# Performance work log

Hardware: AMD Instinct MI355X
Metric: run time of the kernel (lower is better)

Reference implementation:

```python
import jax, jax.numpy as jnp
import numpy as np

B, S, D = 64, 196, 768   # batch, patch-seq, emb_dim
H = 12                   # attention heads
DH = D // H              # 64 per-head dim
HID = 3072               # MLP hidden
NUM_CLASSES = 1000
NUM_ENC = 4              # encoder applied NUM_ENC times with SHARED weights
POS_VOCAB = 201          # nn.Embedding(200+1, D)
EPS = 1e-5


def setup_inputs() -> dict:
    key = jax.random.key(0)
    ks = jax.random.split(key, 16)
    std = 0.02
    return {
        "image": jax.random.normal(ks[0], (B, S, D), jnp.float32),
        "clstoken": jax.random.normal(ks[1], (1, 1, D), jnp.float32),
        "pos_emb": jax.random.normal(ks[2], (POS_VOCAB, D), jnp.float32) * std,
        "ln1_g": jnp.ones((D,), jnp.float32),
        "ln1_b": jnp.zeros((D,), jnp.float32),
        # weights stored [in, out] so y = x @ W (equivalent to torch Linear)
        "wq": jax.random.normal(ks[3], (D, D), jnp.float32) * std,
        "wk": jax.random.normal(ks[4], (D, D), jnp.float32) * std,
        "wv": jax.random.normal(ks[5], (D, D), jnp.float32) * std,
        "ln2_g": jnp.ones((D,), jnp.float32),
        "ln2_b": jnp.zeros((D,), jnp.float32),
        "w1": jax.random.normal(ks[6], (D, HID), jnp.float32) * std,
        "b1": jnp.zeros((HID,), jnp.float32),
        "w2": jax.random.normal(ks[7], (HID, D), jnp.float32) * std,
        "b2": jnp.zeros((D,), jnp.float32),
        "head_w": jax.random.normal(ks[8], (D, NUM_CLASSES), jnp.float32) * std,
        "head_b": jnp.zeros((NUM_CLASSES,), jnp.float32),
    }


def _layernorm(x, g, b):
    mu = jnp.mean(x, axis=-1, keepdims=True)
    var = jnp.mean(jnp.square(x - mu), axis=-1, keepdims=True)
    return (x - mu) * jax.lax.rsqrt(var + EPS) * g + b


def _attention(x, wq, wk, wv):
    b, s, _ = x.shape
    def split_heads(t):  # (b, s, D) -> (b, H, s, DH)
        return t.reshape(b, s, H, DH).transpose(0, 2, 1, 3)
    q = split_heads(x @ wq)
    k = split_heads(x @ wk)
    v = split_heads(x @ wv)
    scores = jnp.einsum("bhqd,bhkd->bhqk", q, k) / np.sqrt(DH).astype(np.float32)
    probs = jax.nn.softmax(scores, axis=-1)
    out = jnp.einsum("bhqk,bhkd->bhqd", probs, v)
    return out.transpose(0, 2, 1, 3).reshape(b, s, D)  # no output projection (as in source)


def _encoder(x, ln1_g, ln1_b, wq, wk, wv, ln2_g, ln2_b, w1, b1, w2, b2):
    a = x + _attention(_layernorm(x, ln1_g, ln1_b), wq, wk, wv)
    h = _layernorm(a, ln2_g, ln2_b)
    mlp = jax.nn.relu(h @ w1 + b1) @ w2 + b2
    return a + mlp


def reference(image, clstoken, pos_emb, ln1_g, ln1_b, wq, wk, wv,
              ln2_g, ln2_b, w1, b1, w2, b2, head_w, head_b):
    b = image.shape[0]
    cls = jnp.broadcast_to(clstoken, (b, 1, D))
    x = jnp.concatenate([cls, image], axis=1)          # (b, S+1, D)
    x = x + pos_emb[: x.shape[1]][None, :, :]           # positional embeddings
    for _ in range(NUM_ENC):                            # shared weights across layers
        x = _encoder(x, ln1_g, ln1_b, wq, wk, wv, ln2_g, ln2_b, w1, b1, w2, b2)
    return x[:, 0, :] @ head_w + head_b                 # (b, num_classes)
```

## Files before the change

### kernel.cpp

```cpp
#include <hip/hip_runtime.h>
#include <hip/hip_bf16.h>
#include <stdint.h>


typedef __attribute__((ext_vector_type(8))) short bf16x8;
typedef __attribute__((ext_vector_type(4))) short bf16x4;
typedef __attribute__((ext_vector_type(4))) float f32x4;

#define LOG2E 1.44269504088896340736f

typedef const __attribute__((address_space(1))) uint32_t gas_u32;
typedef __attribute__((address_space(3))) uint32_t las_u32;

__device__ __forceinline__ void gld_lds16(const void* g, void* l) {
  __builtin_amdgcn_global_load_lds((gas_u32*)g, (las_u32*)l, 16, 0, 0);
}

__device__ __forceinline__ bf16x8 lds_read8u(const __hip_bfloat16* p) {
  union { bf16x4 h[2]; bf16x8 v; } u;
  u.h[0] = *(const bf16x4*)p;
  u.h[1] = *(const bf16x4*)(p + 4);
  return u.v;
}

__device__ __forceinline__ float ldin(const void* p, size_t i, int bf) {
  return bf ? __bfloat162float(((const __hip_bfloat16*)p)[i])
            : ((const float*)p)[i];
}

__device__ __forceinline__ float4 ldin4(const void* p, size_t i4, int bf) {
  if (bf) {
    union { uint2 u; __hip_bfloat16 e[4]; } v;
    v.u = *(const uint2*)((const __hip_bfloat16*)p + i4 * 4);
    return make_float4(__bfloat162float(v.e[0]), __bfloat162float(v.e[1]),
                       __bfloat162float(v.e[2]), __bfloat162float(v.e[3]));
  }
  return ((const float4*)p)[i4];
}

__global__ void k_flag(const void* __restrict__ g, int* __restrict__ flag) {
  if (threadIdx.x == 0 && blockIdx.x == 0) {
    uint32_t w = *(const uint32_t*)g;
    *flag = ((w & 0xFFFFu) == 0x3F80u) ? 1 : 0;
  }
}

__global__ __launch_bounds__(256) void k_embed(
    const void* __restrict__ img, const void* __restrict__ cls,
    const void* __restrict__ pos, float* __restrict__ X,
    const int* __restrict__ dflag)
{
  const int bf = *dflag;
  size_t idx4 = (size_t)blockIdx.x * 256 + threadIdx.x;
  if (idx4 >= (size_t)12608 * 192) return;
  int d4 = (int)(idx4 % 192);
  int row = (int)(idx4 / 192);
  int b = row / 197, s = row % 197;
  float4 base = (s == 0) ? ldin4(cls, d4, bf)
                         : ldin4(img, (size_t)(b * 196 + s - 1) * 192 + d4, bf);
  float4 p = ldin4(pos, (size_t)s * 192 + d4, bf);
  ((float4*)X)[idx4] = make_float4(base.x + p.x, base.y + p.y, base.z + p.z, base.w + p.w);
}

__global__ __launch_bounds__(256) void k_packT(
    const void* __restrict__ in, __hip_bfloat16* __restrict__ out,
    int K, int N, int NR, const int* __restrict__ dflag)
{
  __shared__ float t[32][33];
  const int bf = *dflag;
  int ktiles = (K + 31) >> 5;
  int k0 = (blockIdx.x % ktiles) << 5;
  int n0 = (blockIdx.x / ktiles) << 5;
  int tx = threadIdx.x & 31, ty = threadIdx.x >> 5;
#pragma unroll
  for (int i = 0; i < 32; i += 8) {
    int k = k0 + ty + i, n = n0 + tx;
    t[ty + i][tx] = (k < K && n < N) ? ldin(in, (size_t)k * N + n, bf) : 0.f;
  }
  __syncthreads();
#pragma unroll
  for (int i = 0; i < 32; i += 8) {
    int n = n0 + ty + i, k = k0 + tx;
    if (n < NR && k < K)
      out[(size_t)n * K + k] = __float2bfloat16(t[tx][ty + i]);
  }
}

__global__ __launch_bounds__(256) void k_packcls(
    const float* __restrict__ X, __hip_bfloat16* __restrict__ xcls)
{
  int idx = blockIdx.x * 256 + threadIdx.x;
  if (idx >= 128 * 768) return;
  int r = idx / 768, d = idx % 768;
  float v = (r < 64) ? X[(size_t)r * 197 * 768 + d] : 0.f;
  xcls[idx] = __float2bfloat16(v);
}

__global__ __launch_bounds__(256) void k_ln(
    const float* __restrict__ X, const void* __restrict__ g,
    const void* __restrict__ b, __hip_bfloat16* __restrict__ Y, int rows,
    const int* __restrict__ dflag)
{
  const int bf = *dflag;
  int wave = threadIdx.x >> 6, lane = threadIdx.x & 63;
  int row = blockIdx.x * 4 + wave;
  if (row >= rows) return;
  const float4* xr = (const float4*)(X + (size_t)row * 768);
  float4 v[3];
  float s = 0.f;
#pragma unroll
  for (int i = 0; i < 3; i++) {
    v[i] = xr[lane + i * 64];
    s += v[i].x + v[i].y + v[i].z + v[i].w;
  }
#pragma unroll
  for (int m = 1; m < 64; m <<= 1) s += __shfl_xor(s, m, 64);
  float mu = s * (1.f / 768.f);
  float q = 0.f;
#pragma unroll
  for (int i = 0; i < 3; i++) {
    float dx = v[i].x - mu, dy = v[i].y - mu, dz = v[i].z - mu, dw = v[i].w - mu;
    q += dx * dx + dy * dy + dz * dz + dw * dw;
  }
#pragma unroll
  for (int m = 1; m < 64; m <<= 1) q += __shfl_xor(q, m, 64);
  float rs = rsqrtf(q * (1.f / 768.f) + 1e-5f);
  uint2* yr = (uint2*)(Y + (size_t)row * 768);
#pragma unroll
  for (int i = 0; i < 3; i++) {
    int i4 = lane + i * 64;
    float4 gv = ldin4(g, i4, bf);
    float4 bv = ldin4(b, i4, bf);
    union { uint2 u; __hip_bfloat16 e[4]; } o;
    o.e[0] = __float2bfloat16((v[i].x - mu) * rs * gv.x + bv.x);
    o.e[1] = __float2bfloat16((v[i].y - mu) * rs * gv.y + bv.y);
    o.e[2] = __float2bfloat16((v[i].z - mu) * rs * gv.z + bv.z);
    o.e[3] = __float2bfloat16((v[i].w - mu) * rs * gv.w + bv.w);
    yr[i4] = o.u;
  }
}

template <int EPI>
__global__ __launch_bounds__(256, 2) void k_gemm(
    const __hip_bfloat16* __restrict__ A, const __hip_bfloat16* __restrict__ Bt,
    const void* __restrict__ bias, const float* __restrict__ Res,
    void* __restrict__ Cout, int K, int N, int Mstore, int ntiles,
    const int* __restrict__ dflag)
{
  __shared__ __align__(16) __hip_bfloat16 As[128 * 32];
  __shared__ __align__(16) __hip_bfloat16 Bs[128 * 32];

  const int bf = (EPI == 0) ? 0 : *dflag;
  const int tid = threadIdx.x;
  const int bm = blockIdx.x / ntiles;
  const int bn = blockIdx.x % ntiles;
  const int m0 = bm * 128, n0 = bn * 128;
  const int wave = tid >> 6, lane = tid & 63;
  const int wm = (wave >> 1) * 64, wn = (wave & 1) * 64;
  const int qd = lane >> 4, l16 = lane & 15;

  const int r0 = tid >> 2, kk0 = (tid & 3) * 8;
  const __hip_bfloat16* Ag0 = A + (size_t)(m0 + r0) * K + kk0;
  const __hip_bfloat16* Ag1 = A + (size_t)(m0 + r0 + 64) * K + kk0;
  const __hip_bfloat16* Bg0 = Bt + (size_t)(n0 + r0) * K + kk0;
  const __hip_bfloat16* Bg1 = Bt + (size_t)(n0 + r0 + 64) * K + kk0;
  __hip_bfloat16* As0 = &As[tid * 8];
  __hip_bfloat16* As1 = &As[(tid + 256) * 8];
  __hip_bfloat16* Bs0 = &Bs[tid * 8];
  __hip_bfloat16* Bs1 = &Bs[(tid + 256) * 8];

  f32x4 acc[4][4] = {};

  for (int k0 = 0; k0 < K; k0 += 32) {
    gld_lds16(Ag0, As0); gld_lds16(Ag1, As1);
    gld_lds16(Bg0, Bs0); gld_lds16(Bg1, Bs1);
    Ag0 += 32; Ag1 += 32; Bg0 += 32; Bg1 += 32;
    __syncthreads();
    bf16x8 af[4], bfr[4];
#pragma unroll
    for (int i = 0; i < 4; i++)
      af[i] = *(const bf16x8*)&As[(wm + i * 16 + l16) * 32 + qd * 8];
#pragma unroll
    for (int j = 0; j < 4; j++)
      bfr[j] = *(const bf16x8*)&Bs[(wn + j * 16 + l16) * 32 + qd * 8];
#pragma unroll
    for (int i = 0; i < 4; i++)
#pragma unroll
      for (int j = 0; j < 4; j++)
        acc[i][j] = __builtin_amdgcn_mfma_f32_16x16x32_bf16(af[i], bfr[j], acc[i][j], 0, 0, 0);
    __syncthreads();
  }

#pragma unroll
  for (int i = 0; i < 4; i++) {
#pragma unroll
    for (int r = 0; r < 4; r++) {
      int gr = m0 + wm + i * 16 + qd * 4 + r;
      if (gr < Mstore) {
#pragma unroll
        for (int j = 0; j < 4; j++) {
          int gc = n0 + wn + j * 16 + l16;
          float v = acc[i][j][r];
          if (EPI == 0) {
            ((__hip_bfloat16*)Cout)[(size_t)gr * N + gc] = __float2bfloat16(v);
          } else if (EPI == 1) {
            v += ldin(bias, gc, bf);
            v = v > 0.f ? v : 0.f;
            ((__hip_bfloat16*)Cout)[(size_t)gr * N + gc] = __float2bfloat16(v);
          } else if (EPI == 2) {
            v += ldin(bias, gc, bf) + Res[(size_t)gr * N + gc];
            ((float*)Cout)[(size_t)gr * N + gc] = v;
          } else {
            if (gc < N) {
              v += ldin(bias, gc, bf);
              if (bf) ((__hip_bfloat16*)Cout)[(size_t)gr * N + gc] = __float2bfloat16(v);
              else    ((float*)Cout)[(size_t)gr * N + gc] = v;
            }
          }
        }
      }
    }
  }
}

__global__ __launch_bounds__(256, 2) void k_attn(
    const __hip_bfloat16* __restrict__ qkv,
    const float* __restrict__ X, float* __restrict__ Aout)
{
  const int half = blockIdx.x & 1;
  const int bh = blockIdx.x >> 1;
  const int b = bh / 12, h = bh % 12;
  const size_t tokbase = (size_t)b * 197;

  __shared__ __align__(16) __hip_bfloat16 Ks[128 * 68];
  __shared__ __align__(16) __hip_bfloat16 Vt[64 * 132];
  __shared__ __align__(16) __hip_bfloat16 Ps[4][16 * 132];

  const int tid = threadIdx.x;
  const int wave = tid >> 6, lane = tid & 63;
  const int qd = lane >> 4, l16 = lane & 15;

  const int tbase = half * 7;
  const int tcnt = half ? 6 : 7;
  const int mt[2] = { tbase + wave, tbase + wave + 4 };
  const int nmt = (wave + 4 < tcnt) ? 2 : 1;

  f32x4 Ofr[2][4] = {};
  float mrun[2][4], lrun[2][4];
#pragma unroll
  for (int i = 0; i < 2; i++)
#pragma unroll
    for (int r = 0; r < 4; r++) { mrun[i][r] = -1e30f; lrun[i][r] = 0.f; }

  for (int jt = 0; jt < 2; jt++) {
    const int j0 = jt * 128;
    for (int c = tid; c < 128 * 16; c += 256) {
      int j = c >> 4, ch = (c & 15) * 4;
      const __hip_bfloat16* ksrc = qkv + (tokbase + j0 + j) * 2304 + 768 + h * 64 + ch;
      *(uint2*)&Ks[j * 68 + ch] = *(const uint2*)ksrc;
      const __hip_bfloat16* vsrc = qkv + (tokbase + j0 + j) * 2304 + 1536 + h * 64 + ch;
      union { uint2 u; __hip_bfloat16 e[4]; } vv;
      vv.u = *(const uint2*)vsrc;
      bool jvalid = (j0 + j) < 197;
      __hip_bfloat16 zero = __float2bfloat16(0.f);
#pragma unroll
      for (int i = 0; i < 4; i++)
        Vt[(ch + i) * 132 + j] = jvalid ? vv.e[i] : zero;
    }
    __syncthreads();

#pragma unroll
    for (int im = 0; im < 2; im++) {
      if (im < nmt) {
        const int m0 = mt[im] * 16;
        const __hip_bfloat16* qsrc = qkv + (tokbase + m0 + l16) * 2304 + h * 64 + qd * 8;
        bf16x8 qa0 = *(const bf16x8*)qsrc;
        bf16x8 qa1 = *(const bf16x8*)(qsrc + 32);

        f32x4 sc[8];
#pragma unroll
        for (int nt = 0; nt < 8; nt++) {
          bf16x8 kb0 = lds_read8u(&Ks[(nt * 16 + l16) * 68 + qd * 8]);
          bf16x8 kb1 = lds_read8u(&Ks[(nt * 16 + l16) * 68 + 32 + qd * 8]);
          f32x4 t = {0.f, 0.f, 0.f, 0.f};
          t = __builtin_amdgcn_mfma_f32_16x16x32_bf16(qa0, kb0, t, 0, 0, 0);
          sc[nt] = __builtin_amdgcn_mfma_f32_16x16x32_bf16(qa1, kb1, t, 0, 0, 0);
        }

        float rmax[4];
#pragma unroll
        for (int r = 0; r < 4; r++) rmax[r] = mrun[im][r];
#pragma unroll
        for (int nt = 0; nt < 8; nt++) {
          int col = j0 + nt * 16 + l16;
          bool valid = col < 197;
#pragma unroll
          for (int r = 0; r < 4; r++) {
            float sv = valid ? fminf(fmaxf(sc[nt][r] * 0.125f, -1e30f), 1e30f) : -1e30f;
            sc[nt][r] = sv;
            rmax[r] = fmaxf(rmax[r], sv);
          }
        }
#pragma unroll
        for (int r = 0; r < 4; r++) {
          float v = rmax[r];
          v = fmaxf(v, __shfl_xor(v, 1, 64));
          v = fmaxf(v, __shfl_xor(v, 2, 64));
          v = fmaxf(v, __shfl_xor(v, 4, 64));
          v = fmaxf(v, __shfl_xor(v, 8, 64));
          rmax[r] = v;
        }
        float alpha[4], rsum[4];
#pragma unroll
        for (int r = 0; r < 4; r++) {
          alpha[r] = exp2f((mrun[im][r] - rmax[r]) * LOG2E);
          rsum[r] = 0.f;
        }
#pragma unroll
        for (int nt = 0; nt < 8; nt++) {
#pragma unroll
          for (int r = 0; r < 4; r++) {
            float p = exp2f((sc[nt][r] - rmax[r]) * LOG2E);
            rsum[r] += p;
            Ps[wave][(qd * 4 + r) * 132 + nt * 16 + l16] = __float2bfloat16(p);
          }
        }
#pragma unroll
        for (int r = 0; r < 4; r++) {
          float v = rsum[r];
          v += __shfl_xor(v, 1, 64);
          v += __shfl_xor(v, 2, 64);
          v += __shfl_xor(v, 4, 64);
          v += __shfl_xor(v, 8, 64);
          lrun[im][r] = lrun[im][r] * alpha[r] + v;
          mrun[im][r] = rmax[r];
#pragma unroll
          for (int dt = 0; dt < 4; dt++) Ofr[im][dt][r] *= alpha[r];
        }

#pragma unroll
        for (int kf = 0; kf < 4; kf++) {
          bf16x8 pa = lds_read8u(&Ps[wave][l16 * 132 + kf * 32 + qd * 8]);
#pragma unroll
          for (int dt = 0; dt < 4; dt++) {
            bf16x8 vb = lds_read8u(&Vt[(dt * 16 + l16) * 132 + kf * 32 + qd * 8]);
            Ofr[im][dt] = __builtin_amdgcn_mfma_f32_16x16x32_bf16(pa, vb, Ofr[im][dt], 0, 0, 0);
          }
        }
      }
    }
    __syncthreads();
  }

#pragma unroll
  for (int im = 0; im < 2; im++) {
    if (im < nmt) {
      const int m0 = mt[im] * 16;
#pragma unroll
      for (int r = 0; r < 4; r++) {
        int row = m0 + qd * 4 + r;
        if (row < 197) {
          float inv = 1.f / lrun[im][r];
          size_t gbase = (tokbase + row) * 768 + h * 64;
#pragma unroll
          for (int dt = 0; dt < 4; dt++) {
            int col = dt * 16 + l16;
            Aout[gbase + col] = X[gbase + col] + Ofr[im][dt][r] * inv;
          }
        }
      }
    }
  }
}

extern "C" void kernel_launch(void* const* d_in, const int* in_sizes, int n_in,
                              void* d_out, int out_size, void* d_ws, size_t ws_size,
                              hipStream_t stream)
{
  const void* image = d_in[0];
  const void* cls   = d_in[1];
  const void* pos   = d_in[2];
  const void* ln1g  = d_in[3];
  const void* ln1b  = d_in[4];
  const void* wq    = d_in[5];
  const void* wk    = d_in[6];
  const void* wv    = d_in[7];
  const void* ln2g  = d_in[8];
  const void* ln2b  = d_in[9];
  const void* w1    = d_in[10];
  const void* b1    = d_in[11];
  const void* w2    = d_in[12];
  const void* b2    = d_in[13];
  const void* hw    = d_in[14];
  const void* hb    = d_in[15];

  if (ws_size < 188157952ull) return;

  char* w = (char*)d_ws;
  __hip_bfloat16* xn    = (__hip_bfloat16*)(w);
  __hip_bfloat16* qkv   = (__hip_bfloat16*)(w + 19464192);
  __hip_bfloat16* hid   = qkv;
  __hip_bfloat16* hwT   = qkv;
  __hip_bfloat16* xcls  = (__hip_bfloat16*)(w + 19464192 + 1572864);
  __hip_bfloat16* wqkvT = (__hip_bfloat16*)(w + 97320960);
  __hip_bfloat16* w1T   = (__hip_bfloat16*)(w + 100859904);
  __hip_bfloat16* w2T   = (__hip_bfloat16*)(w + 105578496);
  float* X              = (float*)(w + 110297088);
  float* A              = (float*)(w + 149225472);
  int* dflag            = (int*)(w + 188153856);

  k_flag<<<1, 64, 0, stream>>>(ln1g, dflag);
  k_packT<<<24 * 24, 256, 0, stream>>>(wq, wqkvT,             768,  768,  768, dflag);
  k_packT<<<24 * 24, 256, 0, stream>>>(wk, wqkvT +  768 * 768, 768,  768,  768, dflag);
  k_packT<<<24 * 24, 256, 0, stream>>>(wv, wqkvT + 1536 * 768, 768,  768,  768, dflag);
  k_packT<<<24 * 96, 256, 0, stream>>>(w1, w1T,                768, 3072, 3072, dflag);
  k_packT<<<96 * 24, 256, 0, stream>>>(w2, w2T,               3072,  768,  768, dflag);
  k_embed<<<9456, 256, 0, stream>>>(image, cls, pos, X, dflag);

  for (int l = 0; l < 4; l++) {
    k_ln<<<3152, 256, 0, stream>>>(X, ln1g, ln1b, xn, 12608, dflag);
    k_gemm<0><<<99 * 18, 256, 0, stream>>>(xn, wqkvT, (const void*)nullptr,
                                           (const float*)nullptr, qkv, 768, 2304, 12608, 18, dflag);
    k_attn<<<1536, 256, 0, stream>>>(qkv, X, A);
    k_ln<<<3152, 256, 0, stream>>>(A, ln2g, ln2b, xn, 12608, dflag);
    k_gemm<1><<<99 * 24, 256, 0, stream>>>(xn, w1T, b1, (const float*)nullptr,
                                           hid, 768, 3072, 12608, 24, dflag);
    k_gemm<2><<<99 * 6, 256, 0, stream>>>(hid, w2T, b2, A, X, 3072, 768, 12608, 6, dflag);
  }

  k_packT<<<24 * 32, 256, 0, stream>>>(hw, hwT, 768, 1000, 1024, dflag);
  k_packcls<<<384, 256, 0, stream>>>(X, xcls);
  k_gemm<3><<<8, 256, 0, stream>>>(xcls, hwT, hb, (const float*)nullptr,
                                   d_out, 768, 1000, 64, 8, dflag);
}
```

Measured before the change: 1.601 ms.

## Swizzle GEMM LDS layout and remap blocks to XCDs for L2 reuse

Applies an XOR swizzle to the k-chunk position within each LDS row of the A and B tiles, so the 16-byte fragment reads for MFMA spread across banks instead of conflicting. Remaps block IDs so that consecutive blocks scheduled round-robin across the 8 XCDs share M-tiles within an XCD, which is meant to improve L2 reuse of A rows and weight tiles. The grid is padded to 8*13 M-tiles, and the extra blocks exit early.

```diff
diff --git a/kernel.cpp b/kernel.cpp
--- a/kernel.cpp
+++ b/kernel.cpp
@@ -140,26 +140,37 @@
   }
 }
 
-template <int EPI>
+template <int EPI, int ORDER>
 __global__ __launch_bounds__(256, 2) void k_gemm(
     const __hip_bfloat16* __restrict__ A, const __hip_bfloat16* __restrict__ Bt,
     const void* __restrict__ bias, const float* __restrict__ Res,
-    void* __restrict__ Cout, int K, int N, int Mstore, int ntiles,
+    void* __restrict__ Cout, int K, int N, int Mstore, int ntiles, int mtiles,
     const int* __restrict__ dflag)
 {
   __shared__ __align__(16) __hip_bfloat16 As[128 * 32];
   __shared__ __align__(16) __hip_bfloat16 Bs[128 * 32];
 
+  int bm, bn;
+  if (ORDER == 2) {
+    bm = blockIdx.x / ntiles; bn = blockIdx.x % ntiles;
+  } else {
+    const int xcd = blockIdx.x & 7;
+    const int i = blockIdx.x >> 3;
+    if (ORDER == 0) { bn = i / 13; bm = xcd * 13 + (i % 13); }
+    else            { bm = xcd * 13 + i / ntiles; bn = i % ntiles; }
+    if (bm >= mtiles) return;
+  }
+
   const int bf = (EPI == 0) ? 0 : *dflag;
   const int tid = threadIdx.x;
-  const int bm = blockIdx.x / ntiles;
-  const int bn = blockIdx.x % ntiles;
   const int m0 = bm * 128, n0 = bn * 128;
   const int wave = tid >> 6, lane = tid & 63;
   const int wm = (wave >> 1) * 64, wn = (wave & 1) * 64;
   const int qd = lane >> 4, l16 = lane & 15;
 
-  const int r0 = tid >> 2, kk0 = (tid & 3) * 8;
+  const int r0 = tid >> 2;
+  const int sw0 = (r0 >> 1) & 3;
+  const int kk0 = ((tid & 3) ^ sw0) * 8;
   const __hip_bfloat16* Ag0 = A + (size_t)(m0 + r0) * K + kk0;
   const __hip_bfloat16* Ag1 = A + (size_t)(m0 + r0 + 64) * K + kk0;
   const __hip_bfloat16* Bg0 = Bt + (size_t)(n0 + r0) * K + kk0;
@@ -178,11 +189,15 @@
     __syncthreads();
     bf16x8 af[4], bfr[4];
 #pragma unroll
-    for (int i = 0; i < 4; i++)
-      af[i] = *(const bf16x8*)&As[(wm + i * 16 + l16) * 32 + qd * 8];
-#pragma unroll
-    for (int j = 0; j < 4; j++)
-      bfr[j] = *(const bf16x8*)&Bs[(wn + j * 16 + l16) * 32 + qd * 8];
+    for (int i = 0; i < 4; i++) {
+      int row = wm + i * 16 + l16;
+      af[i] = *(const bf16x8*)&As[row * 32 + ((qd ^ ((row >> 1) & 3)) * 8)];
+    }
+#pragma unroll
+    for (int j = 0; j < 4; j++) {
+      int row = wn + j * 16 + l16;
+      bfr[j] = *(const bf16x8*)&Bs[row * 32 + ((qd ^ ((row >> 1) & 3)) * 8)];
+    }
 #pragma unroll
     for (int i = 0; i < 4; i++)
 #pragma unroll
@@ -410,7 +425,7 @@
   int* dflag            = (int*)(w + 188153856);
 
   k_flag<<<1, 64, 0, stream>>>(ln1g, dflag);
-  k_packT<<<24 * 24, 256, 0, stream>>>(wq, wqkvT,             768,  768,  768, dflag);
+  k_packT<<<24 * 24, 256, 0, stream>>>(wq, wqkvT,              768,  768,  768, dflag);
   k_packT<<<24 * 24, 256, 0, stream>>>(wk, wqkvT +  768 * 768, 768,  768,  768, dflag);
   k_packT<<<24 * 24, 256, 0, stream>>>(wv, wqkvT + 1536 * 768, 768,  768,  768, dflag);
   k_packT<<<24 * 96, 256, 0, stream>>>(w1, w1T,                768, 3072, 3072, dflag);
@@ -419,17 +434,17 @@
 
   for (int l = 0; l < 4; l++) {
     k_ln<<<3152, 256, 0, stream>>>(X, ln1g, ln1b, xn, 12608, dflag);
-    k_gemm<0><<<99 * 18, 256, 0, stream>>>(xn, wqkvT, (const void*)nullptr,
-                                           (const float*)nullptr, qkv, 768, 2304, 12608, 18, dflag);
+    k_gemm<0,0><<<8 * 13 * 18, 256, 0, stream>>>(xn, wqkvT, (const void*)nullptr,
+                                           (const float*)nullptr, qkv, 768, 2304, 12608, 18, 99, dflag);
     k_attn<<<1536, 256, 0, stream>>>(qkv, X, A);
     k_ln<<<3152, 256, 0, stream>>>(A, ln2g, ln2b, xn, 12608, dflag);
-    k_gemm<1><<<99 * 24, 256, 0, stream>>>(xn, w1T, b1, (const float*)nullptr,
-                                           hid, 768, 3072, 12608, 24, dflag);
-    k_gemm<2><<<99 * 6, 256, 0, stream>>>(hid, w2T, b2, A, X, 3072, 768, 12608, 6, dflag);
+    k_gemm<1,0><<<8 * 13 * 24, 256, 0, stream>>>(xn, w1T, b1, (const float*)nullptr,
+                                           hid, 768, 3072, 12608, 24, 99, dflag);
+    k_gemm<2,1><<<8 * 13 * 6, 256, 0, stream>>>(hid, w2T, b2, A, X, 3072, 768, 12608, 6, 99, dflag);
   }
 
   k_packT<<<24 * 32, 256, 0, stream>>>(hw, hwT, 768, 1000, 1024, dflag);
   k_packcls<<<384, 256, 0, stream>>>(X, xcls);
-  k_gemm<3><<<8, 256, 0, stream>>>(xcls, hwT, hb, (const float*)nullptr,
-                                   d_out, 768, 1000, 64, 8, dflag);
-}
+  k_gemm<3,2><<<8, 256, 0, stream>>>(xcls, hwT, hb, (const float*)nullptr,
+                                   d_out, 768, 1000, 64, 8, 1, dflag);
+}
```

New measurement: 1.493 ms. 1.07x faster.
